# Kernel tuning notes

Hardware: AMD Instinct MI355X
Metric: run time of the kernel (lower is better)

## Reference

```python
import jax, jax.numpy as jnp
import numpy as np

B, N, C, K, D, H = 4, 16000, 128, 16, 4, 512
EPS = 1e-5


def _bn(x, g, b, m, v):
    # eval-mode BatchNorm1d over channel dim (applied to flattened B*N rows)
    return (x - m) * jax.lax.rsqrt(v + EPS) * g + b


def _ffn(x, W1, b1, W2, g, b, m, v):
    h = jax.nn.gelu(jnp.einsum('bnc,ch->bnh', x, W1) + b1)
    y = jnp.einsum('bnh,hc->bnc', h, W2)  # second linear has no bias
    return _bn(y, g, b, m, v)


def _vector_feature(x, knn):
    # knn edge max-pooling: max_k ( x[b, knn[b,n,k], :] - x[b, n, :] )
    gathered = jnp.take_along_axis(x[:, :, None, :], knn[:, :, :, None], axis=1)  # (B,N,K,C)
    return jnp.max(gathered - x[:, :, None, :], axis=2)


def _vfr(x, knn, W, g, b, m, v):
    y = jnp.einsum('bnc,cd->bnd', x, W)
    y = _vector_feature(y, knn)
    return _bn(y, g, b, m, v)


def setup_inputs():
    key = jax.random.key(0)
    ks = jax.random.split(key, 16)
    s = 0.05
    return {
        'x': jax.random.normal(ks[0], (B, N, C), jnp.float32),
        'pe': jax.random.normal(ks[1], (B, N, C), jnp.float32),
        'knn': jax.random.randint(ks[2], (B, N, K), 0, N, dtype=jnp.int32),
        # mlp (the single leading FFN)
        'mlp_W1': jax.random.normal(ks[3], (C, H), jnp.float32) * s,
        'mlp_b1': jnp.zeros((H,), jnp.float32),
        'mlp_W2': jax.random.normal(ks[4], (H, C), jnp.float32) * s,
        'mlp_g': jax.random.uniform(ks[5], (C,), jnp.float32, 0.5, 1.5),
        'mlp_beta': jnp.zeros((C,), jnp.float32),
        'mlp_m': jnp.zeros((C,), jnp.float32),
        'mlp_v': jnp.ones((C,), jnp.float32),
        # per-depth VFR params (stacked over depth D)
        'vfr_W': jax.random.normal(ks[6], (D, C, C), jnp.float32) * s,
        'vfr_g': jax.random.uniform(ks[7], (D, C), jnp.float32, 0.5, 1.5),
        'vfr_beta': jnp.zeros((D, C), jnp.float32),
        'vfr_m': jnp.zeros((D, C), jnp.float32),
        'vfr_v': jnp.ones((D, C), jnp.float32),
        # per-depth FFN params
        'ffn_W1': jax.random.normal(ks[8], (D, C, H), jnp.float32) * s,
        'ffn_b1': jnp.zeros((D, H), jnp.float32),
        'ffn_W2': jax.random.normal(ks[9], (D, H, C), jnp.float32) * s,
        'ffn_g': jax.random.uniform(ks[10], (D, C), jnp.float32, 0.5, 1.5),
        'ffn_beta': jnp.zeros((D, C), jnp.float32),
        'ffn_m': jnp.zeros((D, C), jnp.float32),
        'ffn_v': jnp.ones((D, C), jnp.float32),
    }


def reference(x, pe, knn,
              mlp_W1, mlp_b1, mlp_W2, mlp_g, mlp_beta, mlp_m, mlp_v,
              vfr_W, vfr_g, vfr_beta, vfr_m, vfr_v,
              ffn_W1, ffn_b1, ffn_W2, ffn_g, ffn_beta, ffn_m, ffn_v):
    # drop_path is identity in eval mode
    x = x + _ffn(x, mlp_W1, mlp_b1, mlp_W2, mlp_g, mlp_beta, mlp_m, mlp_v)
    for i in range(D):
        x = x + pe
        x = x + _vfr(x, knn, vfr_W[i], vfr_g[i], vfr_beta[i], vfr_m[i], vfr_v[i])
        x = x + _ffn(x, ffn_W1[i], ffn_b1[i], ffn_W2[i], ffn_g[i], ffn_beta[i], ffn_m[i], ffn_v[i])
    return x
```

## Files before the change

### kernel.cpp

```cpp
#include <hip/hip_runtime.h>
#include <hip/hip_bf16.h>

typedef __attribute__((ext_vector_type(8))) short bf16x8;
typedef __attribute__((ext_vector_type(4))) short bf16x4;
typedef __attribute__((ext_vector_type(4))) float f32x4;

#define B_ 4
#define N_ 16000
#define C_ 128
#define K_ 16
#define D_ 4
#define H_ 512
#define R_ (B_*N_)
#define EPSV 1e-5f

__device__ __forceinline__ ushort f2bf(float f) {
    uint32_t b = __builtin_bit_cast(uint32_t, f);
    b += 0x7fffu + ((b >> 16) & 1u);
    return (ushort)(b >> 16);
}
__device__ __forceinline__ float bf2f(ushort u) {
    return __builtin_bit_cast(float, (uint32_t)u << 16);
}
__device__ __forceinline__ float gelu_fast(float v) {
    float v2 = v * v;
    float u = v * fmaf(0.0356774081f, v2, 0.7978845608f);
    float e = __expf(-2.0f * u);
    return v * __builtin_amdgcn_rcpf(1.0f + e);
}
__device__ __forceinline__ void gll16(const void* g, void* l) {
    __builtin_amdgcn_global_load_lds(
        (__attribute__((address_space(1))) void*)g,
        (__attribute__((address_space(3))) void*)l, 16, 0, 0);
}

__global__ void prep_kernel(
    const float* __restrict__ mlp_W1, const float* __restrict__ mlp_b1,
    const float* __restrict__ mlp_W2, const float* __restrict__ mlp_g,
    const float* __restrict__ mlp_be, const float* __restrict__ mlp_m,
    const float* __restrict__ mlp_v,
    const float* __restrict__ vfr_W, const float* __restrict__ vfr_g,
    const float* __restrict__ vfr_be, const float* __restrict__ vfr_m,
    const float* __restrict__ vfr_v,
    const float* __restrict__ ffn_W1, const float* __restrict__ ffn_b1,
    const float* __restrict__ ffn_W2, const float* __restrict__ ffn_g,
    const float* __restrict__ ffn_be, const float* __restrict__ ffn_m,
    const float* __restrict__ ffn_v,
    ushort* __restrict__ w1t, ushort* __restrict__ w2p, ushort* __restrict__ wvt,
    float* __restrict__ b1a, float* __restrict__ fs, float* __restrict__ fb,
    float* __restrict__ vs, float* __restrict__ vb)
{
    int i = blockIdx.x * 256 + threadIdx.x;
    const int NW = 5 * H_ * C_;
    if (i < NW) {
        int f = i / (H_*C_), e = i % (H_*C_);
        int h = e / C_, c = e % C_;
        const float* src = (f == 0) ? mlp_W1 : ffn_W1 + (size_t)(f-1)*C_*H_;
        w1t[i] = f2bf(src[(size_t)c*H_ + h]);
        return;
    }
    i -= NW;
    if (i < NW) {
        int f = i / (H_*C_), e = i % (H_*C_);
        int c = e / H_, p = e % H_;
        int s = p & 31, lam = s >> 3, j = s & 7;
        int h = (p & ~31) + lam*4 + (j & 3) + ((j >> 2) << 4);
        const float* src = (f == 0) ? mlp_W2 : ffn_W2 + (size_t)(f-1)*H_*C_;
        w2p[i] = f2bf(src[(size_t)h*C_ + c]);
        return;
    }
    i -= NW;
    if (i < D_*C_*C_) {
        int d = i / (C_*C_), e = i % (C_*C_);
        int co = e / C_, k = e % C_;
        wvt[i] = f2bf(vfr_W[(size_t)d*C_*C_ + (size_t)k*C_ + co]);
        return;
    }
    i -= D_*C_*C_;
    if (i < 5*H_) {
        int f = i / H_, h = i % H_;
        b1a[i] = (f == 0) ? mlp_b1[h] : ffn_b1[(f-1)*H_ + h];
        return;
    }
    i -= 5*H_;
    if (i < 5*C_) {
        int f = i / C_, c = i % C_;
        float g  = (f==0) ? mlp_g[c]  : ffn_g[(f-1)*C_ + c];
        float be = (f==0) ? mlp_be[c] : ffn_be[(f-1)*C_ + c];
        float m  = (f==0) ? mlp_m[c]  : ffn_m[(f-1)*C_ + c];
        float v  = (f==0) ? mlp_v[c]  : ffn_v[(f-1)*C_ + c];
        float s = g * rsqrtf(v + EPSV);
        fs[i] = s; fb[i] = be - m * s;
        return;
    }
    i -= 5*C_;
    if (i < D_*C_) {
        float s = vfr_g[i] * rsqrtf(vfr_v[i] + EPSV);
        vs[i] = s; vb[i] = vfr_be[i] - vfr_m[i] * s;
    }
}

template<bool ADD_PE>
__global__ __launch_bounds__(512, 4) void ffn_kernel(
    const float* __restrict__ xin, float* __restrict__ xout,
    const float* __restrict__ pe,
    const ushort* __restrict__ W1t,
    const ushort* __restrict__ W2p,
    const float* __restrict__ b1,
    const float* __restrict__ bns, const float* __restrict__ bnb)
{
    __shared__ __attribute__((aligned(16))) char lds[65536];

    const int tid  = threadIdx.x;
    const int m0   = blockIdx.x * 128;
    const int wv   = tid >> 6;
    const int lane = tid & 63;
    const int lr   = lane & 15;
    const int lh   = lane >> 4;

    bf16x8 xa[4];

    auto stageW = [&](int hc, int buf) {
        char* base = lds + buf * 32768;
        const int h0 = hc * 64;
        #pragma unroll
        for (int i = 0; i < 2; ++i) {
            int row = i*32 + wv*4 + (lane >> 4);
            int cb  = (lane & 15) * 16;
            const char* src = (const char*)(W1t + (size_t)(h0 + row) * C_)
                            + (cb ^ ((row & 7) << 4));
            gll16(src, base + i*8192 + wv*1024);
        }
        #pragma unroll
        for (int i = 0; i < 2; ++i) {
            int row = i*64 + wv*8 + (lane >> 3);
            int cb  = (lane & 7) * 16;
            const char* src = (const char*)(W2p + (size_t)row * H_ + h0)
                            + (cb ^ ((row & 7) << 4));
            gll16(src, base + 16384 + i*8192 + wv*1024);
        }
    };

    stageW(0, 0);

    {
        const float* xrow = xin + (size_t)(m0 + wv*16 + lr) * C_ + lh*8;
        #pragma unroll
        for (int kk = 0; kk < 4; ++kk) {
            float4 v0 = *(const float4*)(xrow + kk*32);
            float4 v1 = *(const float4*)(xrow + kk*32 + 4);
            bf16x8 pk;
            pk[0]=(short)f2bf(v0.x); pk[1]=(short)f2bf(v0.y);
            pk[2]=(short)f2bf(v0.z); pk[3]=(short)f2bf(v0.w);
            pk[4]=(short)f2bf(v1.x); pk[5]=(short)f2bf(v1.y);
            pk[6]=(short)f2bf(v1.z); pk[7]=(short)f2bf(v1.w);
            xa[kk] = pk;
        }
    }

    f32x4 acc2[8];
    #pragma unroll
    for (int i = 0; i < 8; ++i) acc2[i] = (f32x4){0.f,0.f,0.f,0.f};

    __syncthreads();

    for (int hc = 0; hc < 8; ++hc) {
        const int h0  = hc * 64;
        const int buf = hc & 1;
        if (hc < 7) stageW(hc + 1, buf ^ 1);

        char* W1s = lds + buf * 32768;
        char* W2s = W1s + 16384;

        f32x4 acc1[4];
        #pragma unroll
        for (int i = 0; i < 4; ++i) acc1[i] = (f32x4){0.f,0.f,0.f,0.f};
        #pragma unroll
        for (int kk = 0; kk < 4; ++kk) {
            int kb = kk*64 + lh*16;
            #pragma unroll
            for (int nf = 0; nf < 4; ++nf) {
                int rb = nf*16 + lr;
                bf16x8 w1 = *(bf16x8*)(W1s + rb*256 + (kb ^ ((rb&7)<<4)));
                acc1[nf] = __builtin_amdgcn_mfma_f32_16x16x32_bf16(w1, xa[kk], acc1[nf], 0, 0, 0);
            }
        }
        bf16x4 pa[4];
        #pragma unroll
        for (int nf = 0; nf < 4; ++nf) {
            float4 bias = *(const float4*)(b1 + h0 + nf*16 + lh*4);
            bf16x4 p;
            p[0] = (short)f2bf(gelu_fast(acc1[nf][0] + bias.x));
            p[1] = (short)f2bf(gelu_fast(acc1[nf][1] + bias.y));
            p[2] = (short)f2bf(gelu_fast(acc1[nf][2] + bias.z));
            p[3] = (short)f2bf(gelu_fast(acc1[nf][3] + bias.w));
            pa[nf] = p;
        }
        #pragma unroll
        for (int g = 0; g < 2; ++g) {
            bf16x8 af = __builtin_shufflevector(pa[2*g], pa[2*g+1], 0,1,2,3,4,5,6,7);
            int kb = g*64 + lh*16;
            #pragma unroll
            for (int nf = 0; nf < 8; ++nf) {
                int rb = nf*16 + lr;
                bf16x8 w2 = *(bf16x8*)(W2s + rb*128 + (kb ^ ((rb&7)<<4)));
                acc2[nf] = __builtin_amdgcn_mfma_f32_16x16x32_bf16(af, w2, acc2[nf], 0, 0, 0);
            }
        }
        __syncthreads();
    }

    #pragma unroll
    for (int nf = 0; nf < 8; ++nf) {
        int col = nf*16 + lr;
        float s = bns[col], bb = bnb[col];
        #pragma unroll
        for (int j = 0; j < 4; ++j) {
            int row = m0 + wv*16 + lh*4 + j;
            size_t o = (size_t)row * C_ + col;
            float base = xin[o] + (ADD_PE ? pe[o] : 0.0f);
            xout[o] = base + acc2[nf][j] * s + bb;
        }
    }
}

__global__ __launch_bounds__(256, 4) void vfr_gemm_kernel(
    const float* __restrict__ x,
    const ushort* __restrict__ Wvt,
    ushort* __restrict__ tout)
{
    __shared__ __attribute__((aligned(16))) char Ws[32768];

    const int tid  = threadIdx.x;
    const int m0   = blockIdx.x * 64;
    const int wv   = tid >> 6;
    const int lane = tid & 63;
    const int lr   = lane & 15;
    const int lh   = lane >> 4;

    #pragma unroll
    for (int i = 0; i < 8; ++i) {
        int row = i*16 + wv*4 + (lane >> 4);
        int cb  = (lane & 15) * 16;
        const char* src = (const char*)(Wvt + (size_t)row * C_)
                        + (cb ^ ((row & 7) << 4));
        gll16(src, Ws + i*4096 + wv*1024);
    }

    bf16x8 xa[4];
    {
        const float* xrow = x + (size_t)(m0 + wv*16 + lr) * C_ + lh*8;
        #pragma unroll
        for (int kk = 0; kk < 4; ++kk) {
            float4 v0 = *(const float4*)(xrow + kk*32);
            float4 v1 = *(const float4*)(xrow + kk*32 + 4);
            bf16x8 pk;
            pk[0]=(short)f2bf(v0.x); pk[1]=(short)f2bf(v0.y);
            pk[2]=(short)f2bf(v0.z); pk[3]=(short)f2bf(v0.w);
            pk[4]=(short)f2bf(v1.x); pk[5]=(short)f2bf(v1.y);
            pk[6]=(short)f2bf(v1.z); pk[7]=(short)f2bf(v1.w);
            xa[kk] = pk;
        }
    }
    __syncthreads();

    f32x4 acc[8];
    #pragma unroll
    for (int i = 0; i < 8; ++i) acc[i] = (f32x4){0.f,0.f,0.f,0.f};
    #pragma unroll
    for (int kk = 0; kk < 4; ++kk) {
        int kb = kk*64 + lh*16;
        #pragma unroll
        for (int nf = 0; nf < 8; ++nf) {
            int rb = nf*16 + lr;
            bf16x8 b = *(bf16x8*)(Ws + rb*256 + (kb ^ ((rb&7)<<4)));
            acc[nf] = __builtin_amdgcn_mfma_f32_16x16x32_bf16(xa[kk], b, acc[nf], 0, 0, 0);
        }
    }
    #pragma unroll
    for (int nf = 0; nf < 8; ++nf) {
        int col = nf*16 + lr;
        #pragma unroll
        for (int j = 0; j < 4; ++j) {
            int row = m0 + wv*16 + lh*4 + j;
            tout[(size_t)row * C_ + col] = f2bf(acc[nf][j]);
        }
    }
}

__global__ __launch_bounds__(256) void vfr_gather_kernel(
    float* __restrict__ x, const ushort* __restrict__ t,
    const int* __restrict__ knn,
    const float* __restrict__ s, const float* __restrict__ bb)
{
    const int wv   = threadIdx.x >> 6;
    const int lane = threadIdx.x & 63;
    const int p = blockIdx.x * 4 + wv;
    const int b = p / N_;
    const int base = b * N_;
    const int* kp = knn + (size_t)p * K_;
    const uint* trow = (const uint*)t;

    uint cen = trow[(size_t)p * 64 + lane];
    float c0 = bf2f((ushort)(cen & 0xffffu));
    float c1 = bf2f((ushort)(cen >> 16));
    float m0v = -INFINITY, m1v = -INFINITY;
    #pragma unroll
    for (int k = 0; k < K_; ++k) {
        int idx = kp[k];
        uint g = trow[(size_t)(base + idx) * 64 + lane];
        m0v = fmaxf(m0v, bf2f((ushort)(g & 0xffffu)));
        m1v = fmaxf(m1v, bf2f((ushort)(g >> 16)));
    }
    m0v -= c0; m1v -= c1;

    int c = lane * 2;
    float2 sv = *(const float2*)(s + c);
    float2 bv = *(const float2*)(bb + c);
    size_t o = (size_t)p * C_ + c;
    float2 xv = *(const float2*)(x + o);
    xv.x += m0v * sv.x + bv.x;
    xv.y += m1v * sv.y + bv.y;
    *(float2*)(x + o) = xv;
}

extern "C" void kernel_launch(void* const* d_in, const int* in_sizes, int n_in,
                              void* d_out, int out_size, void* d_ws, size_t ws_size,
                              hipStream_t stream) {
    const float* x      = (const float*)d_in[0];
    const float* pe     = (const float*)d_in[1];
    const int*   knn    = (const int*)d_in[2];
    const float* mlp_W1 = (const float*)d_in[3];
    const float* mlp_b1 = (const float*)d_in[4];
    const float* mlp_W2 = (const float*)d_in[5];
    const float* mlp_g  = (const float*)d_in[6];
    const float* mlp_be = (const float*)d_in[7];
    const float* mlp_m  = (const float*)d_in[8];
    const float* mlp_v  = (const float*)d_in[9];
    const float* vfr_W  = (const float*)d_in[10];
    const float* vfr_g  = (const float*)d_in[11];
    const float* vfr_be = (const float*)d_in[12];
    const float* vfr_m  = (const float*)d_in[13];
    const float* vfr_v  = (const float*)d_in[14];
    const float* ffn_W1 = (const float*)d_in[15];
    const float* ffn_b1 = (const float*)d_in[16];
    const float* ffn_W2 = (const float*)d_in[17];
    const float* ffn_g  = (const float*)d_in[18];
    const float* ffn_be = (const float*)d_in[19];
    const float* ffn_m  = (const float*)d_in[20];
    const float* ffn_v  = (const float*)d_in[21];
    float* out = (float*)d_out;

    char* ws = (char*)d_ws;
    ushort* tbuf = (ushort*)ws;  ws += (size_t)R_ * C_ * 2;
    ushort* w1t  = (ushort*)ws;  ws += (size_t)5 * H_ * C_ * 2;
    ushort* w2p  = (ushort*)ws;  ws += (size_t)5 * C_ * H_ * 2;
    ushort* wvt  = (ushort*)ws;  ws += (size_t)D_ * C_ * C_ * 2;
    float*  b1a  = (float*)ws;   ws += (size_t)5 * H_ * 4;
    float*  fs   = (float*)ws;   ws += (size_t)5 * C_ * 4;
    float*  fb   = (float*)ws;   ws += (size_t)5 * C_ * 4;
    float*  vs   = (float*)ws;   ws += (size_t)D_ * C_ * 4;
    float*  vb   = (float*)ws;   ws += (size_t)D_ * C_ * 4;

    const int prep_items = 2*(5*H_*C_) + D_*C_*C_ + 5*H_ + 5*C_ + D_*C_;
    prep_kernel<<<(prep_items + 255) / 256, 256, 0, stream>>>(
        mlp_W1, mlp_b1, mlp_W2, mlp_g, mlp_be, mlp_m, mlp_v,
        vfr_W, vfr_g, vfr_be, vfr_m, vfr_v,
        ffn_W1, ffn_b1, ffn_W2, ffn_g, ffn_be, ffn_m, ffn_v,
        w1t, w2p, wvt, b1a, fs, fb, vs, vb);

    ffn_kernel<true><<<R_/128, 512, 0, stream>>>(
        x, out, pe, w1t, w2p, b1a, fs, fb);

    for (int d = 0; d < D_; ++d) {
        vfr_gemm_kernel<<<R_/64, 256, 0, stream>>>(
            out, wvt + (size_t)d * C_ * C_, tbuf);
        vfr_gather_kernel<<<R_/4, 256, 0, stream>>>(
            out, tbuf, knn, vs + d * C_, vb + d * C_);
        if (d < D_ - 1) {
            ffn_kernel<true><<<R_/128, 512, 0, stream>>>(
                out, out, pe,
                w1t + (size_t)(d+1) * H_ * C_, w2p + (size_t)(d+1) * C_ * H_,
                b1a + (d+1) * H_, fs + (d+1) * C_, fb + (d+1) * C_);
        } else {
            ffn_kernel<false><<<R_/128, 512, 0, stream>>>(
                out, out, pe,
                w1t + (size_t)(d+1) * H_ * C_, w2p + (size_t)(d+1) * C_ * H_,
                b1a + (d+1) * H_, fs + (d+1) * C_, fb + (d+1) * C_);
        }
    }
}
```

Before: 366.2 us.

## Fuse VFR projection GEMM into FFN epilogue and shrink FFN blocks

Folds the per-depth VFR linear projection into the tail of the preceding FFN kernel. The FFN output tile is packed to bf16 in registers and multiplied by a permuted VFR weight staged in LDS, so the separate vfr_gemm launch and its re-read of x from global memory go away. The FFN kernel moves from 512 threads and 128 rows with double-buffered weight staging to 256 threads and 64 rows with a single buffer and two barriers per chunk, which loses the load/compute overlap and doubles weight traffic per row. It also swaps MFMA operand order so each lane holds four consecutive columns, allowing float4 residual loads and stores.

```diff
diff --git a/kernel.cpp b/kernel.cpp
--- a/kernel.cpp
+++ b/kernel.cpp
@@ -46,7 +46,7 @@
     const float* __restrict__ ffn_W2, const float* __restrict__ ffn_g,
     const float* __restrict__ ffn_be, const float* __restrict__ ffn_m,
     const float* __restrict__ ffn_v,
-    ushort* __restrict__ w1t, ushort* __restrict__ w2p, ushort* __restrict__ wvt,
+    ushort* __restrict__ w1t, ushort* __restrict__ w2p, ushort* __restrict__ wvs,
     float* __restrict__ b1a, float* __restrict__ fs, float* __restrict__ fb,
     float* __restrict__ vs, float* __restrict__ vb)
 {
@@ -72,8 +72,10 @@
     i -= NW;
     if (i < D_*C_*C_) {
         int d = i / (C_*C_), e = i % (C_*C_);
-        int co = e / C_, k = e % C_;
-        wvt[i] = f2bf(vfr_W[(size_t)d*C_*C_ + (size_t)k*C_ + co]);
+        int co = e / C_, p = e % C_;
+        int s = p & 31, lam = s >> 3, j = s & 7;
+        int k = (p & ~31) + lam*4 + (j & 3) + ((j >> 2) << 4);
+        wvs[i] = f2bf(vfr_W[(size_t)d*C_*C_ + (size_t)k*C_ + co]);
         return;
     }
     i -= D_*C_*C_;
@@ -100,49 +102,29 @@
     }
 }
 
-template<bool ADD_PE>
-__global__ __launch_bounds__(512, 4) void ffn_kernel(
+template<bool ADD_PE, bool NEXT_T>
+__global__ __launch_bounds__(256, 4) void ffn_kernel(
     const float* __restrict__ xin, float* __restrict__ xout,
     const float* __restrict__ pe,
     const ushort* __restrict__ W1t,
     const ushort* __restrict__ W2p,
     const float* __restrict__ b1,
-    const float* __restrict__ bns, const float* __restrict__ bnb)
+    const float* __restrict__ bns, const float* __restrict__ bnb,
+    const ushort* __restrict__ Wvs,
+    ushort* __restrict__ tout)
 {
-    __shared__ __attribute__((aligned(16))) char lds[65536];
+    __shared__ __attribute__((aligned(16))) char lds[32768];
+    char* W1s = lds;
+    char* W2s = lds + 16384;
 
     const int tid  = threadIdx.x;
-    const int m0   = blockIdx.x * 128;
+    const int m0   = blockIdx.x * 64;
     const int wv   = tid >> 6;
     const int lane = tid & 63;
     const int lr   = lane & 15;
     const int lh   = lane >> 4;
 
     bf16x8 xa[4];
-
-    auto stageW = [&](int hc, int buf) {
-        char* base = lds + buf * 32768;
-        const int h0 = hc * 64;
-        #pragma unroll
-        for (int i = 0; i < 2; ++i) {
-            int row = i*32 + wv*4 + (lane >> 4);
-            int cb  = (lane & 15) * 16;
-            const char* src = (const char*)(W1t + (size_t)(h0 + row) * C_)
-                            + (cb ^ ((row & 7) << 4));
-            gll16(src, base + i*8192 + wv*1024);
-        }
-        #pragma unroll
-        for (int i = 0; i < 2; ++i) {
-            int row = i*64 + wv*8 + (lane >> 3);
-            int cb  = (lane & 7) * 16;
-            const char* src = (const char*)(W2p + (size_t)row * H_ + h0)
-                            + (cb ^ ((row & 7) << 4));
-            gll16(src, base + 16384 + i*8192 + wv*1024);
-        }
-    };
-
-    stageW(0, 0);
-
     {
         const float* xrow = xin + (size_t)(m0 + wv*16 + lr) * C_ + lh*8;
         #pragma unroll
@@ -162,15 +144,24 @@
     #pragma unroll
     for (int i = 0; i < 8; ++i) acc2[i] = (f32x4){0.f,0.f,0.f,0.f};
 
-    __syncthreads();
-
     for (int hc = 0; hc < 8; ++hc) {
-        const int h0  = hc * 64;
-        const int buf = hc & 1;
-        if (hc < 7) stageW(hc + 1, buf ^ 1);
-
-        char* W1s = lds + buf * 32768;
-        char* W2s = W1s + 16384;
+        const int h0 = hc * 64;
+        __syncthreads();
+        #pragma unroll
+        for (int i = 0; i < 4; ++i) {
+            int row = i*16 + wv*4 + (lane >> 4);
+            const char* src = (const char*)(W1t + (size_t)(h0 + row) * C_)
+                            + (((lane & 15) * 16) ^ ((row & 7) << 4));
+            gll16(src, W1s + i*4096 + wv*1024);
+        }
+        #pragma unroll
+        for (int i = 0; i < 4; ++i) {
+            int row = i*32 + wv*8 + (lane >> 3);
+            const char* src = (const char*)(W2p + (size_t)row * H_ + h0)
+                            + (((lane & 7) * 16) ^ ((row & 7) << 4));
+            gll16(src, W2s + i*4096 + wv*1024);
+        }
+        __syncthreads();
 
         f32x4 acc1[4];
         #pragma unroll
@@ -204,86 +195,72 @@
             for (int nf = 0; nf < 8; ++nf) {
                 int rb = nf*16 + lr;
                 bf16x8 w2 = *(bf16x8*)(W2s + rb*128 + (kb ^ ((rb&7)<<4)));
-                acc2[nf] = __builtin_amdgcn_mfma_f32_16x16x32_bf16(af, w2, acc2[nf], 0, 0, 0);
+                acc2[nf] = __builtin_amdgcn_mfma_f32_16x16x32_bf16(w2, af, acc2[nf], 0, 0, 0);
             }
         }
+    }
+
+    if (NEXT_T) {
         __syncthreads();
-    }
-
+        #pragma unroll
+        for (int i = 0; i < 8; ++i) {
+            int r = i*16 + wv*4 + (lane >> 4);
+            const char* src = (const char*)(Wvs + (size_t)r * C_)
+                            + (((lane & 15) * 16) ^ ((r & 7) << 4));
+            gll16(src, lds + i*4096 + wv*1024);
+        }
+    }
+
+    const int row = m0 + wv*16 + lr;
+    bf16x4 pa2[8];
     #pragma unroll
     for (int nf = 0; nf < 8; ++nf) {
-        int col = nf*16 + lr;
-        float s = bns[col], bb = bnb[col];
-        #pragma unroll
-        for (int j = 0; j < 4; ++j) {
-            int row = m0 + wv*16 + lh*4 + j;
-            size_t o = (size_t)row * C_ + col;
-            float base = xin[o] + (ADD_PE ? pe[o] : 0.0f);
-            xout[o] = base + acc2[nf][j] * s + bb;
-        }
-    }
-}
-
-__global__ __launch_bounds__(256, 4) void vfr_gemm_kernel(
-    const float* __restrict__ x,
-    const ushort* __restrict__ Wvt,
-    ushort* __restrict__ tout)
-{
-    __shared__ __attribute__((aligned(16))) char Ws[32768];
-
-    const int tid  = threadIdx.x;
-    const int m0   = blockIdx.x * 64;
-    const int wv   = tid >> 6;
-    const int lane = tid & 63;
-    const int lr   = lane & 15;
-    const int lh   = lane >> 4;
-
-    #pragma unroll
-    for (int i = 0; i < 8; ++i) {
-        int row = i*16 + wv*4 + (lane >> 4);
-        int cb  = (lane & 15) * 16;
-        const char* src = (const char*)(Wvt + (size_t)row * C_)
-                        + (cb ^ ((row & 7) << 4));
-        gll16(src, Ws + i*4096 + wv*1024);
-    }
-
-    bf16x8 xa[4];
-    {
-        const float* xrow = x + (size_t)(m0 + wv*16 + lr) * C_ + lh*8;
-        #pragma unroll
-        for (int kk = 0; kk < 4; ++kk) {
-            float4 v0 = *(const float4*)(xrow + kk*32);
-            float4 v1 = *(const float4*)(xrow + kk*32 + 4);
-            bf16x8 pk;
-            pk[0]=(short)f2bf(v0.x); pk[1]=(short)f2bf(v0.y);
-            pk[2]=(short)f2bf(v0.z); pk[3]=(short)f2bf(v0.w);
-            pk[4]=(short)f2bf(v1.x); pk[5]=(short)f2bf(v1.y);
-            pk[6]=(short)f2bf(v1.z); pk[7]=(short)f2bf(v1.w);
-            xa[kk] = pk;
-        }
-    }
-    __syncthreads();
-
-    f32x4 acc[8];
-    #pragma unroll
-    for (int i = 0; i < 8; ++i) acc[i] = (f32x4){0.f,0.f,0.f,0.f};
-    #pragma unroll
-    for (int kk = 0; kk < 4; ++kk) {
-        int kb = kk*64 + lh*16;
+        int c0 = nf*16 + lh*4;
+        float4 sv = *(const float4*)(bns + c0);
+        float4 bv = *(const float4*)(bnb + c0);
+        float4 xi = *(const float4*)(xin + (size_t)row * C_ + c0);
+        if (ADD_PE) {
+            float4 pv = *(const float4*)(pe + (size_t)row * C_ + c0);
+            xi.x += pv.x; xi.y += pv.y; xi.z += pv.z; xi.w += pv.w;
+        }
+        float4 xo;
+        xo.x = xi.x + acc2[nf][0] * sv.x + bv.x;
+        xo.y = xi.y + acc2[nf][1] * sv.y + bv.y;
+        xo.z = xi.z + acc2[nf][2] * sv.z + bv.z;
+        xo.w = xi.w + acc2[nf][3] * sv.w + bv.w;
+        *(float4*)(xout + (size_t)row * C_ + c0) = xo;
+        if (NEXT_T) {
+            bf16x4 p;
+            p[0] = (short)f2bf(xo.x); p[1] = (short)f2bf(xo.y);
+            p[2] = (short)f2bf(xo.z); p[3] = (short)f2bf(xo.w);
+            pa2[nf] = p;
+        }
+    }
+
+    if (NEXT_T) {
+        __syncthreads();
+        f32x4 acc3[8];
+        #pragma unroll
+        for (int i = 0; i < 8; ++i) acc3[i] = (f32x4){0.f,0.f,0.f,0.f};
+        #pragma unroll
+        for (int g = 0; g < 4; ++g) {
+            bf16x8 af = __builtin_shufflevector(pa2[2*g], pa2[2*g+1], 0,1,2,3,4,5,6,7);
+            int kb = g*64 + lh*16;
+            #pragma unroll
+            for (int nf = 0; nf < 8; ++nf) {
+                int rb = nf*16 + lr;
+                bf16x8 b = *(bf16x8*)(lds + rb*256 + (kb ^ ((rb&7)<<4)));
+                acc3[nf] = __builtin_amdgcn_mfma_f32_16x16x32_bf16(af, b, acc3[nf], 0, 0, 0);
+            }
+        }
         #pragma unroll
         for (int nf = 0; nf < 8; ++nf) {
-            int rb = nf*16 + lr;
-            bf16x8 b = *(bf16x8*)(Ws + rb*256 + (kb ^ ((rb&7)<<4)));
-            acc[nf] = __builtin_amdgcn_mfma_f32_16x16x32_bf16(xa[kk], b, acc[nf], 0, 0, 0);
-        }
-    }
-    #pragma unroll
-    for (int nf = 0; nf < 8; ++nf) {
-        int col = nf*16 + lr;
-        #pragma unroll
-        for (int j = 0; j < 4; ++j) {
-            int row = m0 + wv*16 + lh*4 + j;
-            tout[(size_t)row * C_ + col] = f2bf(acc[nf][j]);
+            int col = nf*16 + lr;
+            #pragma unroll
+            for (int j = 0; j < 4; ++j) {
+                int trow = m0 + wv*16 + lh*4 + j;
+                tout[(size_t)trow * C_ + col] = f2bf(acc3[nf][j]);
+            }
         }
     }
 }
@@ -355,7 +332,7 @@
     ushort* tbuf = (ushort*)ws;  ws += (size_t)R_ * C_ * 2;
     ushort* w1t  = (ushort*)ws;  ws += (size_t)5 * H_ * C_ * 2;
     ushort* w2p  = (ushort*)ws;  ws += (size_t)5 * C_ * H_ * 2;
-    ushort* wvt  = (ushort*)ws;  ws += (size_t)D_ * C_ * C_ * 2;
+    ushort* wvs  = (ushort*)ws;  ws += (size_t)D_ * C_ * C_ * 2;
     float*  b1a  = (float*)ws;   ws += (size_t)5 * H_ * 4;
     float*  fs   = (float*)ws;   ws += (size_t)5 * C_ * 4;
     float*  fb   = (float*)ws;   ws += (size_t)5 * C_ * 4;
@@ -367,26 +344,26 @@
         mlp_W1, mlp_b1, mlp_W2, mlp_g, mlp_be, mlp_m, mlp_v,
         vfr_W, vfr_g, vfr_be, vfr_m, vfr_v,
         ffn_W1, ffn_b1, ffn_W2, ffn_g, ffn_be, ffn_m, ffn_v,
-        w1t, w2p, wvt, b1a, fs, fb, vs, vb);
-
-    ffn_kernel<true><<<R_/128, 512, 0, stream>>>(
-        x, out, pe, w1t, w2p, b1a, fs, fb);
+        w1t, w2p, wvs, b1a, fs, fb, vs, vb);
+
+    ffn_kernel<true, true><<<R_/64, 256, 0, stream>>>(
+        x, out, pe, w1t, w2p, b1a, fs, fb, wvs, tbuf);
 
     for (int d = 0; d < D_; ++d) {
-        vfr_gemm_kernel<<<R_/64, 256, 0, stream>>>(
-            out, wvt + (size_t)d * C_ * C_, tbuf);
         vfr_gather_kernel<<<R_/4, 256, 0, stream>>>(
             out, tbuf, knn, vs + d * C_, vb + d * C_);
         if (d < D_ - 1) {
-            ffn_kernel<true><<<R_/128, 512, 0, stream>>>(
+            ffn_kernel<true, true><<<R_/64, 256, 0, stream>>>(
                 out, out, pe,
                 w1t + (size_t)(d+1) * H_ * C_, w2p + (size_t)(d+1) * C_ * H_,
-                b1a + (d+1) * H_, fs + (d+1) * C_, fb + (d+1) * C_);
+                b1a + (d+1) * H_, fs + (d+1) * C_, fb + (d+1) * C_,
+                wvs + (size_t)(d+1) * C_ * C_, tbuf);
         } else {
-            ffn_kernel<false><<<R_/128, 512, 0, stream>>>(
+            ffn_kernel<false, false><<<R_/64, 256, 0, stream>>>(
                 out, out, pe,
                 w1t + (size_t)(d+1) * H_ * C_, w2p + (size_t)(d+1) * C_ * H_,
-                b1a + (d+1) * H_, fs + (d+1) * C_, fb + (d+1) * C_);
-        }
-    }
-}
+                b1a + (d+1) * H_, fs + (d+1) * C_, fb + (d+1) * C_,
+                wvs, tbuf);
+        }
+    }
+}
```

Measured after the change: 350.9 us. 1.04x faster.
